# Kernel tuning notes

Hardware: AMD Instinct MI355X
Metric: run time of the kernel (lower is better)

Reference implementation:

```python
import jax, jax.numpy as jnp
import numpy as np

N = 100000          # nodes
E = 600000          # edges (avg degree ~6, mesh graph)
C_IN = 6            # input features (xyz + normals)
H = 64              # hidden channels per PointTransformerConv
OUT = 10            # out_channels
NEG_SLOPE = 0.01    # F.leaky_relu default slope
IN_DIMS = [C_IN, C_IN + H, C_IN + 2 * H, C_IN + 3 * H]


def _lin(key, fin, fout):
    return jax.random.normal(key, (fin, fout), jnp.float32) / np.float32(np.sqrt(fin))


def setup_inputs() -> dict:
    key = jax.random.key(0)
    ks = jax.random.split(key, 40)
    inp = {
        "x": jax.random.normal(ks[0], (N, C_IN), jnp.float32),
        "edge_index": jax.random.randint(ks[1], (2, E), 0, N, jnp.int32),
    }
    k = 2
    for l, fin in enumerate(IN_DIMS, start=1):
        inp[f"w{l}_lin"] = _lin(ks[k], fin, H); k += 1   # value projection (bias=False)
        inp[f"w{l}_src"] = _lin(ks[k], fin, H); k += 1   # attention src projection
        inp[f"w{l}_dst"] = _lin(ks[k], fin, H); k += 1   # attention dst projection
        inp[f"w{l}_pos"] = _lin(ks[k], fin, H); k += 1   # positional MLP (Linear)
        inp[f"b{l}_pos"] = jnp.zeros((H,), jnp.float32)
    inp["w_mlp1"] = _lin(ks[k], C_IN + 4 * H, H); k += 1
    inp["b_mlp1"] = jnp.zeros((H,), jnp.float32)
    inp["w_mlp2"] = _lin(ks[k], H, OUT); k += 1
    inp["b_mlp2"] = jnp.zeros((OUT,), jnp.float32)
    return inp


def _ptconv(x, src, dst, w_lin, w_src, w_dst, w_pos, b_pos):
    """PointTransformerConv with x serving as both features and positions.
    message = softmax_i(a_dst[i] - a_src[j] + delta_ij) * (h[j] + delta_ij),
    delta_ij = pos_nn(x_i - x_j); sum-aggregated over incoming edges."""
    h = x @ w_lin                                   # [N,H] values
    a_src = x @ w_src                               # [N,H]
    a_dst = x @ w_dst                               # [N,H]
    delta = (x[dst] - x[src]) @ w_pos + b_pos       # [E,H] pos_nn(pos_i - pos_j)
    alpha = a_dst[dst] - a_src[src] + delta         # [E,H] per-edge, per-channel logits
    # numerically stable segment softmax over edges grouped by destination node
    amax = jax.ops.segment_max(alpha, dst, num_segments=N)      # [N,H]
    e = jnp.exp(alpha - amax[dst])                              # [E,H]
    denom = jax.ops.segment_sum(e, dst, num_segments=N)         # [N,H]
    w = e / (denom[dst] + 1e-16)                                # [E,H]
    return jax.ops.segment_sum(w * (h[src] + delta), dst, num_segments=N)  # [N,H]


def _forward(x, edge_index, ps):
    src, dst = edge_index[0], edge_index[1]
    lrelu = lambda v: jnp.where(v > 0, v, NEG_SLOPE * v)
    x1 = _ptconv(x, src, dst, *ps[0])
    x2 = lrelu(_ptconv(jnp.concatenate([x, x1], 1), src, dst, *ps[1]))
    x3 = lrelu(_ptconv(jnp.concatenate([x, x1, x2], 1), src, dst, *ps[2]))
    x4 = lrelu(_ptconv(jnp.concatenate([x, x1, x2, x3], 1), src, dst, *ps[3]))
    out = jnp.concatenate([x, x1, x2, x3, x4], 1)   # [N, 262]
    w_mlp1, b_mlp1, w_mlp2, b_mlp2 = ps[4]
    out = out @ w_mlp1 + b_mlp1                     # dropout = identity (eval mode)
    return out @ w_mlp2 + b_mlp2                    # [N, OUT]


def reference(x, edge_index,
              w1_lin, w1_src, w1_dst, w1_pos, b1_pos,
              w2_lin, w2_src, w2_dst, w2_pos, b2_pos,
              w3_lin, w3_src, w3_dst, w3_pos, b3_pos,
              w4_lin, w4_src, w4_dst, w4_pos, b4_pos,
              w_mlp1, b_mlp1, w_mlp2, b_mlp2):
    ps = [(w1_lin, w1_src, w1_dst, w1_pos, b1_pos),
          (w2_lin, w2_src, w2_dst, w2_pos, b2_pos),
          (w3_lin, w3_src, w3_dst, w3_pos, b3_pos),
          (w4_lin, w4_src, w4_dst, w4_pos, b4_pos),
          (w_mlp1, b_mlp1, w_mlp2, b_mlp2)]
    return _forward(x, edge_index, ps)
```

## Files before the change

kernel.cpp:

```cpp
#include <hip/hip_runtime.h>
#include <hip/hip_fp16.h>

#define NN 100000
#define EE 600000
#define XSB 288
#define SCAN_B 2048
#define LOG2E 1.44269504f

typedef __attribute__((ext_vector_type(8))) short s16x8;
typedef __attribute__((ext_vector_type(4))) float f32x4;

__device__ inline unsigned short f2b(float f) {
    unsigned u = __float_as_uint(f);
    u += 0x7fffu + ((u >> 16) & 1u);
    return (unsigned short)(u >> 16);
}

__device__ inline void accum4(float* d, float* s, const uint4& r) {
    const unsigned* u = (const unsigned*)&r;
#pragma unroll
    for (int ch = 0; ch < 4; ch++) {
        d[ch] += __uint_as_float(u[ch] << 16);
        s[ch] += __uint_as_float(u[ch] & 0xFFFF0000u);
    }
}

__device__ inline void wconv_elem(int idx, int fin,
                                  const float* wlin, const float* wsrc,
                                  const float* wpos, unsigned short* wt) {
    int ks = idx / 6144;
    int rem = idx - ks * 6144;
    int col = rem >> 5, kk = rem & 31;
    int k = ks * 32 + kk;
    int row = (k < 6) ? k : k - 26;
    float val = 0.f;
    if (k < 6 || (k >= 32 && row < fin)) {
        int m = col >> 6, c = col & 63;
        const float* W = (m == 0) ? wlin : (m == 1) ? wsrc : wpos;
        val = W[row * 64 + c];
    }
    wt[idx] = f2b(val);
}

#define O0 1600000
#define O1 1606144
#define O2 1624576
#define O3 1655296
#define O4 1698304
#define O5 1716736
#define O6 2316736
#define O7 2316800

__global__ __launch_bounds__(256) void k_setup(
    const float* __restrict__ x, const int* __restrict__ ei,
    const float* __restrict__ wl0, const float* __restrict__ ws0, const float* __restrict__ wp0,
    const float* __restrict__ wl1, const float* __restrict__ ws1, const float* __restrict__ wp1,
    const float* __restrict__ wl2, const float* __restrict__ ws2, const float* __restrict__ wp2,
    const float* __restrict__ wl3, const float* __restrict__ ws3, const float* __restrict__ wp3,
    const float* __restrict__ w1,
    unsigned short* __restrict__ xb,
    unsigned short* __restrict__ wt0, unsigned short* __restrict__ wt1,
    unsigned short* __restrict__ wt2, unsigned short* __restrict__ wt3,
    unsigned short* __restrict__ w1t, int* __restrict__ deg,
    unsigned* __restrict__ vg) {
    int i = blockIdx.x * 256 + threadIdx.x;
    if (i < O0) {
        int n = i >> 4, c = (i & 15) * 2;
        unsigned lo = (c < 6)     ? (unsigned)f2b(x[n * 6 + c])     : 0u;
        unsigned hi = (c + 1 < 6) ? (unsigned)f2b(x[n * 6 + c + 1]) : 0u;
        *(unsigned*)&xb[(size_t)n * XSB + c] = lo | (hi << 16);
    } else if (i < O1) {
        wconv_elem(i - O0, 6, wl0, ws0, wp0, wt0);
    } else if (i < O2) {
        wconv_elem(i - O1, 70, wl1, ws1, wp1, wt1);
    } else if (i < O3) {
        wconv_elem(i - O2, 134, wl2, ws2, wp2, wt2);
    } else if (i < O4) {
        wconv_elem(i - O3, 198, wl3, ws3, wp3, wt3);
    } else if (i < O5) {
        int idx = i - O4;
        int col = idx / 288, k = idx - col * 288;
        int row = (k < 6) ? k : k - 26;
        bool valid = (k < 6) || (k >= 32 && row < 262);
        w1t[idx] = f2b(valid ? w1[row * 64 + col] : 0.f);
    } else if (i < O6) {
        atomicAdd(&deg[ei[EE + (i - O5)]], 1);
    } else if (i < O7) {
        vg[(size_t)NN * 64 + (i - O6)] = 0u;
    }
}


__global__ void k_scan1(const int* __restrict__ deg, int* __restrict__ rowptr,
                        int* __restrict__ bsum) {
    __shared__ int sh[256];
    int b = blockIdx.x, t = threadIdx.x;
    int base = b * SCAN_B + t * 8;
    int vals[8];
    int s = 0;
#pragma unroll
    for (int j = 0; j < 8; j++) {
        int i = base + j;
        int d = (i < NN) ? deg[i] : 0;
        s += d;
        vals[j] = s;
    }
    sh[t] = s;
    __syncthreads();
    for (int off = 1; off < 256; off <<= 1) {
        int vv = (t >= off) ? sh[t - off] : 0;
        __syncthreads();
        sh[t] += vv;
        __syncthreads();
    }
    int excl = (t > 0) ? sh[t - 1] : 0;
#pragma unroll
    for (int j = 0; j < 8; j++) {
        int i = base + j;
        if (i < NN) rowptr[i + 1] = vals[j] + excl;
    }
    if (t == 255) bsum[b] = sh[255];
}

__global__ void k_scan3m(const int* __restrict__ deg, int* __restrict__ rowptr,
                         const int* __restrict__ bsum, int* __restrict__ cursor) {
    __shared__ int soff;
    int b = blockIdx.x, t = threadIdx.x;
    if (t < 64) {
        int v = (t < b) ? bsum[t] : 0;
#pragma unroll
        for (int m = 1; m < 64; m <<= 1) v += __shfl_xor(v, m);
        if (t == 0) soff = v;
    }
    __syncthreads();
    int off = soff;
    int base = b * SCAN_B + t * 8;
#pragma unroll
    for (int j = 0; j < 8; j++) {
        int i = base + j;
        if (i < NN) {
            int incl = rowptr[i + 1] + off;
            rowptr[i + 1] = incl;
            cursor[i] = incl - deg[i];
        }
    }
    if (b == 0 && t == 0) rowptr[0] = 0;
}

__global__ void k_scatter(const int* __restrict__ ei, int* __restrict__ cursor,
                          int* __restrict__ csrc) {
    int e = blockIdx.x * 256 + threadIdx.x;
    if (e < EE) {
        int d = ei[EE + e];
        int pos = atomicAdd(&cursor[d], 1);
        csrc[pos] = ei[e];
    }
}


template <int KP>
__global__ __launch_bounds__(256) void k_projm(
    const unsigned short* __restrict__ xb, const unsigned short* __restrict__ wt,
    const float* __restrict__ bpos,
    unsigned* __restrict__ vg, __half* __restrict__ qh) {
    __shared__ short wl[192 * 32];
    const int t = threadIdx.x;
    const int w = t >> 6, l = t & 63;
    const int lo = l & 15, hi = l >> 4;
    const int row_w = blockIdx.x * 128 + w * 32;

    f32x4 acc[2][12];
#pragma unroll
    for (int a = 0; a < 2; a++)
#pragma unroll
        for (int i = 0; i < 12; i++) acc[a][i] = (f32x4)0.f;

    const unsigned short* arow0 = xb + (size_t)(row_w + lo) * XSB;
    const unsigned short* arow1 = xb + (size_t)(row_w + 16 + lo) * XSB;
#pragma unroll
    for (int ks = 0; ks < KP / 32; ks++) {
        __syncthreads();
        {
            const uint4* src = (const uint4*)wt + (size_t)ks * 768;
            uint4* dst = (uint4*)wl;
#pragma unroll
            for (int i = 0; i < 3; i++) {
                int idx = i * 256 + t;
                dst[idx ^ ((idx >> 3) & 7)] = src[idx];
            }
        }
        __syncthreads();
        s16x8 af0 = *(const s16x8*)(arow0 + ks * 32 + hi * 8);
        s16x8 af1 = *(const s16x8*)(arow1 + ks * 32 + hi * 8);
#pragma unroll
        for (int ct = 0; ct < 12; ct++) {
            int ridx = (ct * 16 + lo) * 4 + hi;
            s16x8 bf = *(const s16x8*)&wl[(size_t)(ridx ^ ((ridx >> 3) & 7)) * 8];
            acc[0][ct] = __builtin_amdgcn_mfma_f32_16x16x32_bf16(af0, bf, acc[0][ct], 0, 0, 0);
            acc[1][ct] = __builtin_amdgcn_mfma_f32_16x16x32_bf16(af1, bf, acc[1][ct], 0, 0, 0);
        }
    }

#pragma unroll
    for (int tile = 0; tile < 2; tile++) {
#pragma unroll
        for (int r = 0; r < 4; r++) {
            int node = row_w + tile * 16 + hi * 4 + r;
            if (node < NN) {
#pragma unroll
                for (int j = 0; j < 4; j++) {
                    int c = j * 16 + lo;
                    float h  = acc[tile][0 + j][r];
                    float as = acc[tile][4 + j][r];
                    float p  = acc[tile][8 + j][r];
                    size_t o = (size_t)node * 64 + c;
                    float P = __builtin_amdgcn_exp2f(-(as + p) * LOG2E);
                    vg[o] = (unsigned)f2b(P) | ((unsigned)f2b(P * (h - p)) << 16);
                    qh[o] = __float2half(p + bpos[c]);
                }
            }
        }
    }
}


__global__ __launch_bounds__(256) void k_mlp1f(
    const unsigned short* __restrict__ xb, const unsigned short* __restrict__ w1t,
    const float* __restrict__ b1, const float* __restrict__ w2,
    const float* __restrict__ b2, float* __restrict__ out) {
    __shared__ float w2l[64][10];
    __shared__ float b2l[10];
    __shared__ float b1l[64];
    for (int t = threadIdx.x; t < 714; t += 256) {
        if (t < 640) ((float*)w2l)[t] = w2[t];
        else if (t < 650) b2l[t - 640] = b2[t - 640];
        else b1l[t - 650] = b1[t - 650];
    }
    __syncthreads();

    const int w = threadIdx.x >> 6, l = threadIdx.x & 63;
    const int lo = l & 15, hi = l >> 4;
    const int row_w = blockIdx.x * 256 + w * 64;

    f32x4 acc[4][4];
#pragma unroll
    for (int a = 0; a < 4; a++)
#pragma unroll
        for (int b = 0; b < 4; b++) acc[a][b] = (f32x4)0.f;

#pragma unroll
    for (int ks = 0; ks < 9; ks++) {
        const int k0 = ks * 32 + hi * 8;
        s16x8 bf[4];
#pragma unroll
        for (int ct = 0; ct < 4; ct++)
            bf[ct] = *(const s16x8*)(w1t + (size_t)(ct * 16 + lo) * 288 + k0);
#pragma unroll
        for (int rt = 0; rt < 4; rt++) {
            s16x8 af = *(const s16x8*)(xb + (size_t)(row_w + rt * 16 + lo) * XSB + k0);
#pragma unroll
            for (int ct = 0; ct < 4; ct++)
                acc[rt][ct] = __builtin_amdgcn_mfma_f32_16x16x32_bf16(af, bf[ct], acc[rt][ct], 0, 0, 0);
        }
    }

#pragma unroll
    for (int rt = 0; rt < 4; rt++) {
#pragma unroll
        for (int r = 0; r < 4; r++) {
            int node = row_w + rt * 16 + hi * 4 + r;
            float po[10];
#pragma unroll
            for (int o = 0; o < 10; o++) po[o] = 0.f;
#pragma unroll
            for (int ct = 0; ct < 4; ct++) {
                int c = ct * 16 + lo;
                float hv = acc[rt][ct][r] + b1l[c];
#pragma unroll
                for (int o = 0; o < 10; o++) po[o] = fmaf(hv, w2l[c][o], po[o]);
            }
#pragma unroll
            for (int m = 1; m < 16; m <<= 1)
#pragma unroll
                for (int o = 0; o < 10; o++) po[o] += __shfl_xor(po[o], m);
            if (lo == 0 && node < NN) {
                float* op = out + (size_t)node * 10;
#pragma unroll
                for (int o = 0; o < 5; o++)
                    *(float2*)(op + o * 2) = make_float2(po[o * 2] + b2l[o * 2],
                                                         po[o * 2 + 1] + b2l[o * 2 + 1]);
            }
        }
    }
}


template <int RELU>
__global__ __launch_bounds__(256) void k_edge(
    const uint4* __restrict__ vg,
    const uint2* __restrict__ qh,
    const int* __restrict__ rowptr, const int* __restrict__ csrc,
    unsigned short* __restrict__ xb, int col) {
    int l = threadIdx.x & 63;
    int g = l >> 4, lg = l & 15, gbase = g * 16;
    int node = (blockIdx.x * 4 + (threadIdx.x >> 6)) * 4 + g;
    int b = rowptr[node], e = rowptr[node + 1];
    int deg = e - b;
    int pre = csrc[b + lg];
    uint2 qr = qh[(size_t)node * 16 + lg];
    float d[4] = {0.f, 0.f, 0.f, 0.f};
    float s[4] = {0.f, 0.f, 0.f, 0.f};

    {
        int idx[8];
#pragma unroll
        for (int k = 0; k < 8; k++)
            idx[k] = (k < deg) ? __shfl(pre, gbase + k) : NN;
        uint4 r[8];
#pragma unroll
        for (int k = 0; k < 8; k++) r[k] = vg[(size_t)idx[k] * 16 + lg];
#pragma unroll
        for (int k = 0; k < 8; k++) accum4(d, s, r[k]);
    }
    if (deg > 8) {
        int idx[8];
#pragma unroll
        for (int k = 0; k < 8; k++)
            idx[k] = (8 + k < deg) ? __shfl(pre, gbase + 8 + k) : NN;
        uint4 r[8];
#pragma unroll
        for (int k = 0; k < 8; k++) r[k] = vg[(size_t)idx[k] * 16 + lg];
#pragma unroll
        for (int k = 0; k < 8; k++) accum4(d, s, r[k]);
        for (int it = 16; it < deg; ++it) {
            uint4 r0 = vg[(size_t)csrc[b + it] * 16 + lg];
            accum4(d, s, r0);
        }
    }

    float2 q01 = __half22float2(*(const __half2*)&qr.x);
    float2 q23 = __half22float2(*(const __half2*)&qr.y);
    float qv[4] = {q01.x, q01.y, q23.x, q23.y};
    float o[4];
#pragma unroll
    for (int ch = 0; ch < 4; ch++) {
        float v = (s[ch] + qv[ch] * d[ch]) / (d[ch] + 1e-16f);
        if (RELU) v = (v > 0.f) ? v : 0.01f * v;
        o[ch] = v;
    }
    unsigned p01 = (unsigned)f2b(o[0]) | ((unsigned)f2b(o[1]) << 16);
    unsigned p23 = (unsigned)f2b(o[2]) | ((unsigned)f2b(o[3]) << 16);
    *(uint2*)(xb + (size_t)node * XSB + col + 4 * lg) = make_uint2(p01, p23);
}


extern "C" void kernel_launch(void* const* d_in, const int* in_sizes, int n_in,
                              void* d_out, int out_size, void* d_ws, size_t ws_size,
                              hipStream_t stream) {
    const float* x = (const float*)d_in[0];
    const int* ei = (const int*)d_in[1];
    const float* W[4][4];
    const float* BP[4];
    int base = 2;
    for (int l = 0; l < 4; l++) {
        for (int m = 0; m < 4; m++) W[l][m] = (const float*)d_in[base + m];
        BP[l] = (const float*)d_in[base + 4];
        base += 5;
    }
    const float* w1 = (const float*)d_in[22];
    const float* b1 = (const float*)d_in[23];
    const float* w2 = (const float*)d_in[24];
    const float* b2 = (const float*)d_in[25];

    char* wsp = (char*)d_ws;
    size_t off = 0;
    auto alloc = [&](size_t bytes) {
        void* p = wsp + off;
        off += (bytes + 255) & ~(size_t)255;
        return p;
    };
    unsigned short* xb = (unsigned short*)alloc((size_t)(NN + 256) * XSB * 2);
    unsigned* vg = (unsigned*)alloc((size_t)(NN + 1) * 64 * 4);
    __half* qh = (__half*)alloc((size_t)NN * 64 * 2);
    int* deg = (int*)alloc((size_t)NN * 4);
    int* rowptr = (int*)alloc((size_t)(NN + 1) * 4);
    int* cursor = (int*)alloc((size_t)NN * 4);
    int* bsum = (int*)alloc(1024 * 4);
    int* csrc = (int*)alloc((size_t)(EE + 16) * 4);
    const int KPv[4] = {32, 96, 160, 224};
    unsigned short* wt[4];
    for (int l = 0; l < 4; l++) wt[l] = (unsigned short*)alloc((size_t)192 * KPv[l] * 2);
    unsigned short* w1t = (unsigned short*)alloc((size_t)64 * 288 * 2);

    hipMemsetAsync(deg, 0, (size_t)NN * 4, stream);
    k_setup<<<(O7 + 255) / 256, 256, 0, stream>>>(
        x, ei,
        W[0][0], W[0][1], W[0][3],
        W[1][0], W[1][1], W[1][3],
        W[2][0], W[2][1], W[2][3],
        W[3][0], W[3][1], W[3][3], w1,
        xb, wt[0], wt[1], wt[2], wt[3], w1t, deg, vg);

    int nb = (NN + SCAN_B - 1) / SCAN_B;
    k_scan1<<<nb, 256, 0, stream>>>(deg, rowptr, bsum);
    k_scan3m<<<nb, 256, 0, stream>>>(deg, rowptr, bsum, cursor);
    k_scatter<<<(EE + 255) / 256, 256, 0, stream>>>(ei, cursor, csrc);

    const int gProj = (NN + 127) / 128;
    const int gEdge = NN / 16;
    const uint4* vgu = (const uint4*)vg;
    const uint2* qh2 = (const uint2*)qh;

    k_projm<32><<<gProj, 256, 0, stream>>>(xb, wt[0], BP[0], vg, qh);
    k_edge<0><<<gEdge, 256, 0, stream>>>(vgu, qh2, rowptr, csrc, xb, 32);
    k_projm<96><<<gProj, 256, 0, stream>>>(xb, wt[1], BP[1], vg, qh);
    k_edge<1><<<gEdge, 256, 0, stream>>>(vgu, qh2, rowptr, csrc, xb, 96);
    k_projm<160><<<gProj, 256, 0, stream>>>(xb, wt[2], BP[2], vg, qh);
    k_edge<1><<<gEdge, 256, 0, stream>>>(vgu, qh2, rowptr, csrc, xb, 160);
    k_projm<224><<<gProj, 256, 0, stream>>>(xb, wt[3], BP[3], vg, qh);
    k_edge<1><<<gEdge, 256, 0, stream>>>(vgu, qh2, rowptr, csrc, xb, 224);

    k_mlp1f<<<(NN + 255) / 256, 256, 0, stream>>>(xb, w1t, b1, w2, b2, (float*)d_out);
}
```

Measured before the change: 293.4 us.

## Fuse edge aggregation of layer l with projection of layer l+1

Adds a fused kernel in which each block first aggregates edges for its 64 nodes, writing the layer output into the bf16 feature buffer, and then immediately runs the MFMA projection for the next layer on those same rows. The vg/qh buffers become double-buffered so the next layer's projections can be written while the current layer's are still being read. This removes three kernel launches and lets the freshly written feature rows be reread from cache, at the cost of a 16-row-per-wave MFMA tile and less parallelism inside the projection phase.

New measurement: 307.3 us. 4.7% more time.

```diff
diff --git a/kernel.cpp b/kernel.cpp
--- a/kernel.cpp
+++ b/kernel.cpp
@@ -49,7 +49,7 @@
 #define O4 1698304
 #define O5 1716736
 #define O6 2316736
-#define O7 2316800
+#define O7 2316864
 
 __global__ __launch_bounds__(256) void k_setup(
     const float* __restrict__ x, const int* __restrict__ ei,
@@ -62,7 +62,7 @@
     unsigned short* __restrict__ wt0, unsigned short* __restrict__ wt1,
     unsigned short* __restrict__ wt2, unsigned short* __restrict__ wt3,
     unsigned short* __restrict__ w1t, int* __restrict__ deg,
-    unsigned* __restrict__ vg) {
+    unsigned* __restrict__ vg0, unsigned* __restrict__ vg1) {
     int i = blockIdx.x * 256 + threadIdx.x;
     if (i < O0) {
         int n = i >> 4, c = (i & 15) * 2;
@@ -86,7 +86,9 @@
     } else if (i < O6) {
         atomicAdd(&deg[ei[EE + (i - O5)]], 1);
     } else if (i < O7) {
-        vg[(size_t)NN * 64 + (i - O6)] = 0u;
+        int j = i - O6;
+        unsigned* dst = (j < 64) ? vg0 : vg1;
+        dst[(size_t)NN * 64 + (j & 63)] = 0u;
     }
 }
 
@@ -155,6 +157,71 @@
         int pos = atomicAdd(&cursor[d], 1);
         csrc[pos] = ei[e];
     }
+}
+
+
+template <int RELU>
+__device__ inline void edge_node(
+    int node, int lg, int gbase, int pre, int deg, int b,
+    const uint4* __restrict__ vgA, const uint2* __restrict__ qhA,
+    const int* __restrict__ csrc, unsigned short* __restrict__ xb, int col) {
+    uint2 qr = qhA[(size_t)node * 16 + lg];
+    float d[4] = {0.f, 0.f, 0.f, 0.f};
+    float s[4] = {0.f, 0.f, 0.f, 0.f};
+    {
+        int idx[8];
+#pragma unroll
+        for (int k = 0; k < 8; k++)
+            idx[k] = (k < deg) ? __shfl(pre, gbase + k) : NN;
+        uint4 r[8];
+#pragma unroll
+        for (int k = 0; k < 8; k++) r[k] = vgA[(size_t)idx[k] * 16 + lg];
+#pragma unroll
+        for (int k = 0; k < 8; k++) accum4(d, s, r[k]);
+    }
+    if (deg > 8) {
+        int idx[8];
+#pragma unroll
+        for (int k = 0; k < 8; k++)
+            idx[k] = (8 + k < deg) ? __shfl(pre, gbase + 8 + k) : NN;
+        uint4 r[8];
+#pragma unroll
+        for (int k = 0; k < 8; k++) r[k] = vgA[(size_t)idx[k] * 16 + lg];
+#pragma unroll
+        for (int k = 0; k < 8; k++) accum4(d, s, r[k]);
+        for (int it = 16; it < deg; ++it) {
+            uint4 r0 = vgA[(size_t)csrc[b + it] * 16 + lg];
+            accum4(d, s, r0);
+        }
+    }
+    float2 q01 = __half22float2(*(const __half2*)&qr.x);
+    float2 q23 = __half22float2(*(const __half2*)&qr.y);
+    float qv[4] = {q01.x, q01.y, q23.x, q23.y};
+    float o[4];
+#pragma unroll
+    for (int ch = 0; ch < 4; ch++) {
+        float v = (s[ch] + qv[ch] * d[ch]) / (d[ch] + 1e-16f);
+        if (RELU) v = (v > 0.f) ? v : 0.01f * v;
+        o[ch] = v;
+    }
+    unsigned p01 = (unsigned)f2b(o[0]) | ((unsigned)f2b(o[1]) << 16);
+    unsigned p23 = (unsigned)f2b(o[2]) | ((unsigned)f2b(o[3]) << 16);
+    *(uint2*)(xb + (size_t)node * XSB + col + 4 * lg) = make_uint2(p01, p23);
+}
+
+
+template <int RELU>
+__global__ __launch_bounds__(256) void k_edge(
+    const uint4* __restrict__ vg, const uint2* __restrict__ qh,
+    const int* __restrict__ rowptr, const int* __restrict__ csrc,
+    unsigned short* __restrict__ xb, int col) {
+    int l = threadIdx.x & 63;
+    int g = l >> 4, lg = l & 15, gbase = g * 16;
+    int node = (blockIdx.x * 4 + (threadIdx.x >> 6)) * 4 + g;
+    int b = rowptr[node], e = rowptr[node + 1];
+    int deg = e - b;
+    int pre = csrc[b + lg];
+    edge_node<RELU>(node, lg, gbase, pre, deg, b, vg, qh, csrc, xb, col);
 }
 
 
@@ -224,6 +291,81 @@
 }
 
 
+template <int KP, int RELU>
+__global__ __launch_bounds__(256) void k_edgeproj(
+    const uint4* __restrict__ vgA, const uint2* __restrict__ qhA,
+    const int* __restrict__ rowptr, const int* __restrict__ csrc,
+    unsigned short* __restrict__ xb, int col,
+    const unsigned short* __restrict__ wt, const float* __restrict__ bpos,
+    unsigned* __restrict__ vgB, __half* __restrict__ qhB) {
+    __shared__ short wl[192 * 32];
+    const int t = threadIdx.x;
+    const int w = t >> 6, l = t & 63;
+    const int lo = l & 15, hi = l >> 4;
+    const int g = l >> 4, lg = l & 15, gbase = g * 16;
+    const int gi = w * 4 + g;
+    const int row0 = blockIdx.x * 64;
+
+#pragma unroll 1
+    for (int j = 0; j < 4; ++j) {
+        int node = row0 + j * 16 + gi;
+        if (node < NN) {
+            int b = rowptr[node], e = rowptr[node + 1];
+            int deg = e - b;
+            int pre = csrc[b + lg];
+            edge_node<RELU>(node, lg, gbase, pre, deg, b, vgA, qhA, csrc, xb, col);
+        }
+    }
+    __syncthreads();
+
+    const int row_w = row0 + w * 16;
+    f32x4 acc[12];
+#pragma unroll
+    for (int i = 0; i < 12; i++) acc[i] = (f32x4)0.f;
+
+    const unsigned short* arow = xb + (size_t)(row_w + lo) * XSB;
+#pragma unroll
+    for (int ks = 0; ks < KP / 32; ks++) {
+        __syncthreads();
+        {
+            const uint4* src = (const uint4*)wt + (size_t)ks * 768;
+            uint4* dst = (uint4*)wl;
+#pragma unroll
+            for (int i = 0; i < 3; i++) {
+                int idx = i * 256 + t;
+                dst[idx ^ ((idx >> 3) & 7)] = src[idx];
+            }
+        }
+        __syncthreads();
+        s16x8 af = *(const s16x8*)(arow + ks * 32 + hi * 8);
+#pragma unroll
+        for (int ct = 0; ct < 12; ct++) {
+            int ridx = (ct * 16 + lo) * 4 + hi;
+            s16x8 bf = *(const s16x8*)&wl[(size_t)(ridx ^ ((ridx >> 3) & 7)) * 8];
+            acc[ct] = __builtin_amdgcn_mfma_f32_16x16x32_bf16(af, bf, acc[ct], 0, 0, 0);
+        }
+    }
+
+#pragma unroll
+    for (int r = 0; r < 4; r++) {
+        int node = row_w + hi * 4 + r;
+        if (node < NN) {
+#pragma unroll
+            for (int j = 0; j < 4; j++) {
+                int c = j * 16 + lo;
+                float h  = acc[0 + j][r];
+                float as = acc[4 + j][r];
+                float p  = acc[8 + j][r];
+                size_t o = (size_t)node * 64 + c;
+                float P = __builtin_amdgcn_exp2f(-(as + p) * LOG2E);
+                vgB[o] = (unsigned)f2b(P) | ((unsigned)f2b(P * (h - p)) << 16);
+                qhB[o] = __float2half(p + bpos[c]);
+            }
+        }
+    }
+}
+
+
 __global__ __launch_bounds__(256) void k_mlp1f(
     const unsigned short* __restrict__ xb, const unsigned short* __restrict__ w1t,
     const float* __restrict__ b1, const float* __restrict__ w2,
@@ -292,65 +434,6 @@
             }
         }
     }
-}
-
-
-template <int RELU>
-__global__ __launch_bounds__(256) void k_edge(
-    const uint4* __restrict__ vg,
-    const uint2* __restrict__ qh,
-    const int* __restrict__ rowptr, const int* __restrict__ csrc,
-    unsigned short* __restrict__ xb, int col) {
-    int l = threadIdx.x & 63;
-    int g = l >> 4, lg = l & 15, gbase = g * 16;
-    int node = (blockIdx.x * 4 + (threadIdx.x >> 6)) * 4 + g;
-    int b = rowptr[node], e = rowptr[node + 1];
-    int deg = e - b;
-    int pre = csrc[b + lg];
-    uint2 qr = qh[(size_t)node * 16 + lg];
-    float d[4] = {0.f, 0.f, 0.f, 0.f};
-    float s[4] = {0.f, 0.f, 0.f, 0.f};
-
-    {
-        int idx[8];
-#pragma unroll
-        for (int k = 0; k < 8; k++)
-            idx[k] = (k < deg) ? __shfl(pre, gbase + k) : NN;
-        uint4 r[8];
-#pragma unroll
-        for (int k = 0; k < 8; k++) r[k] = vg[(size_t)idx[k] * 16 + lg];
-#pragma unroll
-        for (int k = 0; k < 8; k++) accum4(d, s, r[k]);
-    }
-    if (deg > 8) {
-        int idx[8];
-#pragma unroll
-        for (int k = 0; k < 8; k++)
-            idx[k] = (8 + k < deg) ? __shfl(pre, gbase + 8 + k) : NN;
-        uint4 r[8];
-#pragma unroll
-        for (int k = 0; k < 8; k++) r[k] = vg[(size_t)idx[k] * 16 + lg];
-#pragma unroll
-        for (int k = 0; k < 8; k++) accum4(d, s, r[k]);
-        for (int it = 16; it < deg; ++it) {
-            uint4 r0 = vg[(size_t)csrc[b + it] * 16 + lg];
-            accum4(d, s, r0);
-        }
-    }
-
-    float2 q01 = __half22float2(*(const __half2*)&qr.x);
-    float2 q23 = __half22float2(*(const __half2*)&qr.y);
-    float qv[4] = {q01.x, q01.y, q23.x, q23.y};
-    float o[4];
-#pragma unroll
-    for (int ch = 0; ch < 4; ch++) {
-        float v = (s[ch] + qv[ch] * d[ch]) / (d[ch] + 1e-16f);
-        if (RELU) v = (v > 0.f) ? v : 0.01f * v;
-        o[ch] = v;
-    }
-    unsigned p01 = (unsigned)f2b(o[0]) | ((unsigned)f2b(o[1]) << 16);
-    unsigned p23 = (unsigned)f2b(o[2]) | ((unsigned)f2b(o[3]) << 16);
-    *(uint2*)(xb + (size_t)node * XSB + col + 4 * lg) = make_uint2(p01, p23);
 }
 
 
@@ -380,8 +463,10 @@
         return p;
     };
     unsigned short* xb = (unsigned short*)alloc((size_t)(NN + 256) * XSB * 2);
-    unsigned* vg = (unsigned*)alloc((size_t)(NN + 1) * 64 * 4);
-    __half* qh = (__half*)alloc((size_t)NN * 64 * 2);
+    unsigned* vg0 = (unsigned*)alloc((size_t)(NN + 1) * 64 * 4);
+    unsigned* vg1 = (unsigned*)alloc((size_t)(NN + 1) * 64 * 4);
+    __half* qh0 = (__half*)alloc((size_t)NN * 64 * 2);
+    __half* qh1 = (__half*)alloc((size_t)NN * 64 * 2);
     int* deg = (int*)alloc((size_t)NN * 4);
     int* rowptr = (int*)alloc((size_t)(NN + 1) * 4);
     int* cursor = (int*)alloc((size_t)NN * 4);
@@ -399,7 +484,7 @@
         W[1][0], W[1][1], W[1][3],
         W[2][0], W[2][1], W[2][3],
         W[3][0], W[3][1], W[3][3], w1,
-        xb, wt[0], wt[1], wt[2], wt[3], w1t, deg, vg);
+        xb, wt[0], wt[1], wt[2], wt[3], w1t, deg, vg0, vg1);
 
     int nb = (NN + SCAN_B - 1) / SCAN_B;
     k_scan1<<<nb, 256, 0, stream>>>(deg, rowptr, bsum);
@@ -407,18 +492,18 @@
     k_scatter<<<(EE + 255) / 256, 256, 0, stream>>>(ei, cursor, csrc);
 
     const int gProj = (NN + 127) / 128;
+    const int gFuse = (NN + 63) / 64;
     const int gEdge = NN / 16;
-    const uint4* vgu = (const uint4*)vg;
-    const uint2* qh2 = (const uint2*)qh;
-
-    k_projm<32><<<gProj, 256, 0, stream>>>(xb, wt[0], BP[0], vg, qh);
-    k_edge<0><<<gEdge, 256, 0, stream>>>(vgu, qh2, rowptr, csrc, xb, 32);
-    k_projm<96><<<gProj, 256, 0, stream>>>(xb, wt[1], BP[1], vg, qh);
-    k_edge<1><<<gEdge, 256, 0, stream>>>(vgu, qh2, rowptr, csrc, xb, 96);
-    k_projm<160><<<gProj, 256, 0, stream>>>(xb, wt[2], BP[2], vg, qh);
-    k_edge<1><<<gEdge, 256, 0, stream>>>(vgu, qh2, rowptr, csrc, xb, 160);
-    k_projm<224><<<gProj, 256, 0, stream>>>(xb, wt[3], BP[3], vg, qh);
-    k_edge<1><<<gEdge, 256, 0, stream>>>(vgu, qh2, rowptr, csrc, xb, 224);
+
+    k_projm<32><<<gProj, 256, 0, stream>>>(xb, wt[0], BP[0], vg0, qh0);
+    k_edgeproj<96, 0><<<gFuse, 256, 0, stream>>>(
+        (const uint4*)vg0, (const uint2*)qh0, rowptr, csrc, xb, 32, wt[1], BP[1], vg1, qh1);
+    k_edgeproj<160, 1><<<gFuse, 256, 0, stream>>>(
+        (const uint4*)vg1, (const uint2*)qh1, rowptr, csrc, xb, 96, wt[2], BP[2], vg0, qh0);
+    k_edgeproj<224, 1><<<gFuse, 256, 0, stream>>>(
+        (const uint4*)vg0, (const uint2*)qh0, rowptr, csrc, xb, 160, wt[3], BP[3], vg1, qh1);
+    k_edge<1><<<gEdge, 256, 0, stream>>>(
+        (const uint4*)vg1, (const uint2*)qh1, rowptr, csrc, xb, 224);
 
     k_mlp1f<<<(NN + 255) / 256, 256, 0, stream>>>(xb, w1t, b1, w2, b2, (float*)d_out);
 }
```
